# Performance work log

Hardware: AMD Instinct MI355X
Metric: run time of the kernel (lower is better)

Reference implementation:

```python
import jax, jax.numpy as jnp
import numpy as np

N_RBF = 20
CUTOFF = 5.0
N_BASIS = 128
N_FILTERS = 128
N_LAYERS = 3
B, N = 128, 128
N_PAIRS = 524288


def ssp(x):
    # ShiftedSoftplus: softplus(x) - log(2)
    return jax.nn.softplus(x) - jnp.log(2.0).astype(x.dtype)


def gaussian_rbf(d):
    # schnetpack-style GaussianRBF: offsets in [0, cutoff], shared width
    offsets = jnp.linspace(0.0, CUTOFF, N_RBF, dtype=d.dtype)
    width = offsets[1] - offsets[0]
    coeff = -0.5 / (width * width)
    diff = d[:, None] - offsets[None, :]  # [n_pairs, n_rbf]
    return jnp.exp(coeff * diff * diff)


def cosine_cutoff(d):
    fc = 0.5 * (jnp.cos(d * (jnp.pi / CUTOFF)) + 1.0)
    return fc * (d < CUTOFF).astype(d.dtype)


def setup_inputs() -> dict:
    key = jax.random.key(0)
    ks = jax.random.split(key, 16)
    inp = {
        "Z": jax.random.randint(ks[0], (B, N), 0, 100),
        "R": jax.random.normal(ks[1], (B, N, 3), dtype=jnp.float32) * 2.0,
        "idx_i": jax.random.randint(ks[2], (N_PAIRS,), 0, B * N),
        "idx_j": jax.random.randint(ks[3], (N_PAIRS,), 0, B * N),
        "emb": jax.random.normal(ks[4], (100, N_BASIS), dtype=jnp.float32) * 0.1,
    }
    s = 0.05
    inp["in2f_W"] = jax.random.normal(ks[5], (N_LAYERS, N_BASIS, N_FILTERS), dtype=jnp.float32) * s
    inp["in2f_b"] = jnp.zeros((N_LAYERS, N_FILTERS), dtype=jnp.float32)
    inp["fW1"] = jax.random.normal(ks[6], (N_LAYERS, N_RBF, N_FILTERS), dtype=jnp.float32) * s
    inp["fb1"] = jnp.zeros((N_LAYERS, N_FILTERS), dtype=jnp.float32)
    inp["fW2"] = jax.random.normal(ks[7], (N_LAYERS, N_FILTERS, N_FILTERS), dtype=jnp.float32) * s
    inp["fb2"] = jnp.zeros((N_LAYERS, N_FILTERS), dtype=jnp.float32)
    inp["oW1"] = jax.random.normal(ks[8], (N_LAYERS, N_FILTERS, N_BASIS), dtype=jnp.float32) * s
    inp["ob1"] = jnp.zeros((N_LAYERS, N_BASIS), dtype=jnp.float32)
    inp["oW2"] = jax.random.normal(ks[9], (N_LAYERS, N_BASIS, N_BASIS), dtype=jnp.float32) * s
    inp["ob2"] = jnp.zeros((N_LAYERS, N_BASIS), dtype=jnp.float32)
    return inp


def _interaction(x, f_ij, rcut_ij, idx_i, idx_j, W_in, b_in, fW1, fb1, fW2, fb2, oW1, ob1, oW2, ob2):
    # x: [B, N, n_atom_basis]
    h = jnp.einsum("bnf,fg->bng", x, W_in) + b_in          # input_to_feature
    h = h.reshape(-1, h.shape[-1])                           # [B*N, n_filters]
    # filter network on RBFs
    Wij = ssp(f_ij @ fW1 + fb1) @ fW2 + fb2                  # [n_pairs, n_filters]
    Wij = Wij * rcut_ij[:, None]
    x_ij = h[idx_j] * Wij                                     # gather + multiply
    agg = jax.ops.segment_sum(x_ij, idx_i, num_segments=h.shape[0])  # scatter_add
    out = ssp(agg @ oW1 + ob1) @ oW2 + ob2                    # feature_to_output
    return out.reshape(x.shape[0], x.shape[1], N_BASIS)


def reference(Z, R, idx_i, idx_j, emb, in2f_W, in2f_b, fW1, fb1, fW2, fb2, oW1, ob1, oW2, ob2):
    coords = R.reshape(-1, 3)                                 # [B*N, 3]
    vec = coords[idx_i] - coords[idx_j]
    d_ij = jnp.linalg.norm(vec, axis=-1)                      # [n_pairs]
    f_ij = gaussian_rbf(d_ij)                                 # [n_pairs, 20]
    rcut_ij = cosine_cutoff(d_ij)                             # [n_pairs]
    x = emb[Z]                                                # [B, N, 128]
    for l in range(N_LAYERS):
        v = _interaction(x, f_ij, rcut_ij, idx_i, idx_j,
                         in2f_W[l], in2f_b[l], fW1[l], fb1[l], fW2[l], fb2[l],
                         oW1[l], ob1[l], oW2[l], ob2[l])
        x = x + v
    return x
```

## Files before the change

kernel.cpp:

```cpp
#include <hip/hip_runtime.h>
#include <hip/hip_fp16.h>

#define NPAIRS 524288
#define NATOMS 16384
#define TBINS  2048
#define TROWS  2049
#define CAP    80
#define CUTOFF_F 5.0f

typedef _Float16 f16;
typedef f16 f16x4 __attribute__((ext_vector_type(4)));
typedef f16 f16x8 __attribute__((ext_vector_type(8)));
typedef float f32x4 __attribute__((ext_vector_type(4)));

__device__ __forceinline__ float sspf(float v) {
  float a = fabsf(v);
  return fmaxf(v, 0.0f) + log1pf(expf(-a)) - 0.69314718055994531f;
}

__device__ __forceinline__ int swz(int row, int kh) {
  return (row << 8) + ((kh << 1) ^ ((row & 7) << 4));
}
__device__ __forceinline__ int swzW(int col, int kh) {
  return (col << 7) + ((kh << 1) ^ ((col & 7) << 4));
}

__device__ __forceinline__ uint4 ldtab(const f16* __restrict__ tabL, int v, int c) {
  return *(const uint4*)(tabL + ((unsigned)(v >> 14) << 7) + (c << 3));
}
__device__ __forceinline__ uint4 ldh(const f16* __restrict__ hin, int v, int c) {
  return *(const uint4*)(hin + ((unsigned)(v & 16383) << 7) + (c << 3));
}
__device__ __forceinline__ void dot8(float* acc, uint4 wv, uint4 hv) {
  const __half* wp = (const __half*)&wv;
  const __half* hp = (const __half*)&hv;
  #pragma unroll
  for (int q = 0; q < 8; ++q)
    acc[q] = fmaf(__half2float(wp[q]), __half2float(hp[q]), acc[q]);
}

__global__ __launch_bounds__(256) void prep(const float* __restrict__ fW1,
                                            const float* __restrict__ fb1,
                                            const float* __restrict__ fW2,
                                            const float* __restrict__ fb2,
                                            f16* __restrict__ table,
                                            const float* __restrict__ in2f_W,
                                            const float* __restrict__ oW1,
                                            const float* __restrict__ oW2,
                                            f16* __restrict__ wsw,
                                            int* __restrict__ cursor) {
  __shared__ float hid[8 * 128];
  int t = threadIdx.x;
  int bid = blockIdx.x;

  if (bid >= 843) { cursor[(bid - 843) * 256 + t] = 0; return; }

  if (bid >= 771) {
    int bid2 = bid - 771;
    int mm = bid2 >> 3;
    int tloc = (bid2 & 7) * 256 + t;
    int col = tloc & 127, k0 = (tloc >> 7) << 3;
    const float* src = mm < 3 ? in2f_W + (size_t)mm * 16384
                     : mm < 6 ? oW1 + (size_t)(mm - 3) * 16384
                              : oW2 + (size_t)(mm - 6) * 16384;
    f16x8 v;
    #pragma unroll
    for (int kk = 0; kk < 8; ++kk) v[kk] = (f16)src[(k0 + kk) * 128 + col];
    *(f16x8*)((char*)wsw + (size_t)mm * 32768 + (k0 >> 6) * 16384 + swzW(col, k0 & 63)) = v;
    return;
  }

  int l = bid / 257, rem = bid % 257;
  int e = t >> 5, q = t & 31;
  int ti = rem * 8 + e;
  const float* W1 = fW1 + (size_t)l * 20 * 128;
  const float* B1 = fb1 + (size_t)l * 128;
  const float* W2 = fW2 + (size_t)l * 128 * 128;
  const float* B2 = fb2 + (size_t)l * 128;

  const float width = CUTOFF_F / 19.0f;
  const float coeff = -0.5f / (width * width);
  const float dstep = CUTOFF_F / (float)TBINS;
  float d = (float)ti * dstep;

  float4 h4 = *(const float4*)&B1[q * 4];
  #pragma unroll
  for (int r = 0; r < 20; ++r) {
    float diff = d - (float)r * width;
    float fr = expf(coeff * diff * diff);
    float4 w4 = *(const float4*)&W1[r * 128 + q * 4];
    h4.x += fr * w4.x; h4.y += fr * w4.y; h4.z += fr * w4.z; h4.w += fr * w4.w;
  }
  *(float4*)&hid[e * 128 + q * 4] =
      make_float4(sspf(h4.x), sspf(h4.y), sspf(h4.z), sspf(h4.w));
  __syncthreads();

  float4 o4 = *(const float4*)&B2[q * 4];
  const float4* W2g = (const float4*)W2;
  #pragma unroll 4
  for (int g = 0; g < 128; ++g) {
    float hv = hid[e * 128 + g];
    float4 w4 = W2g[g * 32 + q];
    o4.x += hv * w4.x; o4.y += hv * w4.y; o4.z += hv * w4.z; o4.w += hv * w4.w;
  }

  if (ti < TROWS) {
    float fc = (d < CUTOFF_F) ? 0.5f * (cosf(d * 0.62831853071795865f) + 1.0f) : 0.0f;
    f16x4 hv = { (f16)(o4.x * fc), (f16)(o4.y * fc), (f16)(o4.z * fc), (f16)(o4.w * fc) };
    *(f16x4*)((f16*)table + ((size_t)l * TROWS + ti) * 128 + q * 4) = hv;
  }
}

__global__ __launch_bounds__(256) void pg0(const int* __restrict__ Z,
                                           const float* __restrict__ emb,
                                           const f16* __restrict__ Wsw,
                                           const float* __restrict__ bias,
                                           f16* __restrict__ hout,
                                           const int* __restrict__ idx_i,
                                           const int* __restrict__ idx_j,
                                           const float* __restrict__ R,
                                           int* __restrict__ cursor,
                                           int* __restrict__ pjd) {
  __shared__ char smem[49152];
  char* Al = smem;
  char* Wl = smem + 16384;
  int t = threadIdx.x;

  if (blockIdx.x < 2048) {
    int p = blockIdx.x * 256 + t;
    int i = idx_i[p], j = idx_j[p];
    float dx = R[(size_t)i*3+0] - R[(size_t)j*3+0];
    float dy = R[(size_t)i*3+1] - R[(size_t)j*3+1];
    float dz = R[(size_t)i*3+2] - R[(size_t)j*3+2];
    float d = sqrtf(dx*dx + dy*dy + dz*dz);
    if (d < CUTOFF_F) {
      int bin = __float2int_rn(d * ((float)TBINS / CUTOFF_F));
      int slot = atomicAdd(&cursor[i], 1);
      if (slot < CAP) pjd[i * CAP + slot] = j | (bin << 14);
    }
    return;
  }

  size_t rbase = (size_t)(blockIdx.x - 2048) * 64;
  #pragma unroll
  for (int i = 0; i < 8; ++i) {
    int idx = i * 256 + t;
    int r = idx >> 5, q = idx & 31;
    int z = Z[rbase + r];
    float4 v = ((const float4*)emb)[(size_t)z * 32 + q];
    f16x4 h = { (f16)v.x, (f16)v.y, (f16)v.z, (f16)v.w };
    *(f16x4*)(Al + swz(r, q * 4)) = h;
  }
  #pragma unroll
  for (int i = 0; i < 8; ++i) ((uint4*)Wl)[i * 256 + t] = ((const uint4*)Wsw)[i * 256 + t];
  __syncthreads();

  int w = t >> 6, lane = t & 63;
  int lo = lane & 15, hi = lane >> 4;
  f16x8 fa[4];
  #pragma unroll
  for (int s = 0; s < 4; ++s)
    fa[s] = *(f16x8*)(Al + swz(16 * w + lo, s * 32 + hi * 8));

  #pragma unroll
  for (int cb = 0; cb < 8; ++cb) {
    f32x4 acc = {0.0f, 0.0f, 0.0f, 0.0f};
    #pragma unroll
    for (int s = 0; s < 4; ++s) {
      f16x8 fb = *(f16x8*)(Wl + (s >> 1) * 16384 + swzW(cb * 16 + lo, (s & 1) * 32 + hi * 8));
      acc = __builtin_amdgcn_mfma_f32_16x16x32_f16(fa[s], fb, acc, 0, 0, 0);
    }
    int col = cb * 16 + lo;
    float bc = bias[col];
    #pragma unroll
    for (int j = 0; j < 4; ++j)
      hout[(rbase + 16 * w + hi * 4 + j) * 128 + col] = (f16)(acc[j] + bc);
  }
}

template <int FIRST, int HAS_NEXT>
__global__ __launch_bounds__(512, 8) void aggfuse(const int* __restrict__ pjd,
                                                  const int* __restrict__ cnt,
                                                  const f16* __restrict__ hin,
                                                  const f16* __restrict__ tabL,
                                                  const f16* __restrict__ W1sw,
                                                  const float* __restrict__ ob1,
                                                  const f16* __restrict__ W2sw,
                                                  const float* __restrict__ ob2,
                                                  const int* __restrict__ Z,
                                                  const float* __restrict__ emb,
                                                  float* __restrict__ x,
                                                  const f16* __restrict__ Wnsw,
                                                  const float* __restrict__ bn,
                                                  f16* __restrict__ hout) {
  __shared__ char smem[24576];
  char* Wl  = smem;
  char* AlT = smem + 16384;
  char* Tl  = smem + 20480;
  int tid = threadIdx.x;
  int wv = tid >> 6, lane = tid & 63;
  int s = lane >> 4, c = lane & 15;
  int rbase = blockIdx.x * 16;
  const int S = (TBINS << 14);

  {
    int a = rbase + wv * 2 + (s & 1);
    int half = s >> 1;
    int p0 = a * CAP;
    int n = min(cnt[a], CAP);
    int nh = half * 2;

    int m = (n + 3) >> 2;
    m = max(m, __shfl_xor(m, 16, 64));
    m = max(m, __shfl_xor(m, 32, 64));

    float acc[8];
    #pragma unroll
    for (int q = 0; q < 8; ++q) acc[q] = 0.0f;

    int vA  = (nh < n)     ? pjd[p0 + nh]     : S;
    int vB  = (nh + 1 < n) ? pjd[p0 + nh + 1] : S;
    int vA1 = (nh + 4 < n) ? pjd[p0 + nh + 4] : S;
    int vB1 = (nh + 5 < n) ? pjd[p0 + nh + 5] : S;
    uint4 wA = ldtab(tabL, vA, c), hA = ldh(hin, vA, c);
    uint4 wB = ldtab(tabL, vB, c), hB = ldh(hin, vB, c);

    for (int it = 0; it < m; ++it) {
      int k2 = 4 * (it + 2) + nh;
      int vA2 = (k2 < n)     ? pjd[p0 + k2]     : S;
      int vB2 = (k2 + 1 < n) ? pjd[p0 + k2 + 1] : S;
      uint4 wAn = ldtab(tabL, vA1, c), hAn = ldh(hin, vA1, c);
      uint4 wBn = ldtab(tabL, vB1, c), hBn = ldh(hin, vB1, c);
      dot8(acc, wA, hA);
      dot8(acc, wB, hB);
      wA = wAn; hA = hAn; wB = wBn; hB = hBn;
      vA1 = vA2; vB1 = vB2;
    }

    #pragma unroll
    for (int q = 0; q < 8; ++q) acc[q] += __shfl_xor(acc[q], 32, 64);

    if (s < 2) {
      int row = wv * 2 + s;
      f16x8 pk;
      #pragma unroll
      for (int q = 0; q < 8; ++q) pk[q] = (f16)acc[q];
      *(f16x8*)(AlT + swz(row, c * 8)) = pk;
    }
  }
  __syncthreads();

  int lo = c, hi = s;
  int col = wv * 16 + lo;

  float res[4];
  if (FIRST) {
    #pragma unroll
    for (int j = 0; j < 4; ++j) {
      int z = Z[rbase + hi * 4 + j];
      res[j] = emb[(size_t)z * 128 + col];
    }
  } else {
    #pragma unroll
    for (int j = 0; j < 4; ++j)
      res[j] = x[(size_t)(rbase + hi * 4 + j) * 128 + col];
  }

  {
    f16x8 fa[4];
    #pragma unroll
    for (int ss = 0; ss < 4; ++ss)
      fa[ss] = *(f16x8*)(AlT + swz(lo, ss * 32 + hi * 8));
    f32x4 acc = {0.0f, 0.0f, 0.0f, 0.0f};
    #pragma unroll
    for (int half = 0; half < 2; ++half) {
      #pragma unroll
      for (int i = 0; i < 2; ++i)
        ((uint4*)Wl)[i * 512 + tid] = ((const uint4*)W1sw)[half * 1024 + i * 512 + tid];
      __syncthreads();
      #pragma unroll
      for (int sh = 0; sh < 2; ++sh) {
        int ss = half * 2 + sh;
        f16x8 fb = *(f16x8*)(Wl + swzW(col, sh * 32 + hi * 8));
        acc = __builtin_amdgcn_mfma_f32_16x16x32_f16(fa[ss], fb, acc, 0, 0, 0);
      }
      __syncthreads();
    }
    float bc = ob1[col];
    #pragma unroll
    for (int j = 0; j < 4; ++j)
      *(f16*)(Tl + swz(hi * 4 + j, col)) = (f16)sspf(acc[j] + bc);
  }
  __syncthreads();

  {
    f32x4 acc = {0.0f, 0.0f, 0.0f, 0.0f};
    f16x8 fa[4];
    #pragma unroll
    for (int half = 0; half < 2; ++half) {
      #pragma unroll
      for (int i = 0; i < 2; ++i)
        ((uint4*)Wl)[i * 512 + tid] = ((const uint4*)W2sw)[half * 1024 + i * 512 + tid];
      __syncthreads();
      if (half == 0) {
        #pragma unroll
        for (int ss = 0; ss < 4; ++ss)
          fa[ss] = *(f16x8*)(Tl + swz(lo, ss * 32 + hi * 8));
      }
      #pragma unroll
      for (int sh = 0; sh < 2; ++sh) {
        int ss = half * 2 + sh;
        f16x8 fb = *(f16x8*)(Wl + swzW(col, sh * 32 + hi * 8));
        acc = __builtin_amdgcn_mfma_f32_16x16x32_f16(fa[ss], fb, acc, 0, 0, 0);
      }
      __syncthreads();
    }
    float bc = ob2[col];
    #pragma unroll
    for (int j = 0; j < 4; ++j) {
      int r = hi * 4 + j;
      float xn = res[j] + acc[j] + bc;
      x[(size_t)(rbase + r) * 128 + col] = xn;
      if (HAS_NEXT) *(f16*)(AlT + swz(r, col)) = (f16)xn;
    }
  }

  if (HAS_NEXT) {
    __syncthreads();
    f32x4 acc = {0.0f, 0.0f, 0.0f, 0.0f};
    f16x8 fa[4];
    #pragma unroll
    for (int half = 0; half < 2; ++half) {
      #pragma unroll
      for (int i = 0; i < 2; ++i)
        ((uint4*)Wl)[i * 512 + tid] = ((const uint4*)Wnsw)[half * 1024 + i * 512 + tid];
      __syncthreads();
      if (half == 0) {
        #pragma unroll
        for (int ss = 0; ss < 4; ++ss)
          fa[ss] = *(f16x8*)(AlT + swz(lo, ss * 32 + hi * 8));
      }
      #pragma unroll
      for (int sh = 0; sh < 2; ++sh) {
        int ss = half * 2 + sh;
        f16x8 fb = *(f16x8*)(Wl + swzW(col, sh * 32 + hi * 8));
        acc = __builtin_amdgcn_mfma_f32_16x16x32_f16(fa[ss], fb, acc, 0, 0, 0);
      }
      __syncthreads();
    }
    float bc = bn[col];
    #pragma unroll
    for (int j = 0; j < 4; ++j)
      hout[(size_t)(rbase + hi * 4 + j) * 128 + col] = (f16)(acc[j] + bc);
  }
}

extern "C" void kernel_launch(void* const* d_in, const int* in_sizes, int n_in,
                              void* d_out, int out_size, void* d_ws, size_t ws_size,
                              hipStream_t stream) {
  const int*   Z      = (const int*)d_in[0];
  const float* R      = (const float*)d_in[1];
  const int*   idx_i  = (const int*)d_in[2];
  const int*   idx_j  = (const int*)d_in[3];
  const float* emb    = (const float*)d_in[4];
  const float* in2f_W = (const float*)d_in[5];
  const float* in2f_b = (const float*)d_in[6];
  const float* fW1    = (const float*)d_in[7];
  const float* fb1    = (const float*)d_in[8];
  const float* fW2    = (const float*)d_in[9];
  const float* fb2    = (const float*)d_in[10];
  const float* oW1    = (const float*)d_in[11];
  const float* ob1    = (const float*)d_in[12];
  const float* oW2    = (const float*)d_in[13];
  const float* ob2    = (const float*)d_in[14];
  float* x = (float*)d_out;

  char* ws = (char*)d_ws;
  int*  cursor = (int*) (ws + 0x000000);
  int*  pjd    = (int*) (ws + 0x010000);
  f16*  table  = (f16*) (ws + 0x510000);
  f16*  h0     = (f16*) (ws + 0x6A0000);
  f16*  h1     = (f16*) (ws + 0xAA0000);
  f16*  wsw    = (f16*) (ws + 0xEA0000);

  prep<<<907, 256, 0, stream>>>(fW1, fb1, fW2, fb2, table, in2f_W, oW1, oW2, wsw, cursor);
  pg0<<<2304, 256, 0, stream>>>(Z, emb, wsw, in2f_b, h0, idx_i, idx_j, R, cursor, pjd);

  aggfuse<1, 1><<<NATOMS / 16, 512, 0, stream>>>(pjd, cursor, h0, table + 0 * (size_t)TROWS * 128,
                                                 wsw + 3 * 16384, ob1,
                                                 wsw + 6 * 16384, ob2,
                                                 Z, emb, x,
                                                 wsw + 1 * 16384, in2f_b + 128, h1);
  aggfuse<0, 1><<<NATOMS / 16, 512, 0, stream>>>(pjd, cursor, h1, table + 1 * (size_t)TROWS * 128,
                                                 wsw + 4 * 16384, ob1 + 128,
                                                 wsw + 7 * 16384, ob2 + 128,
                                                 Z, emb, x,
                                                 wsw + 2 * 16384, in2f_b + 256, h0);
  aggfuse<0, 0><<<NATOMS / 16, 512, 0, stream>>>(pjd, cursor, h0, table + 2 * (size_t)TROWS * 128,
                                                 wsw + 5 * 16384, ob1 + 256,
                                                 wsw + 8 * 16384, ob2 + 256,
                                                 Z, emb, x, nullptr, nullptr, nullptr);
}
```

Before: 120.4 us.

## Read MFMA weight fragments from global memory and double aggfuse block size

The staging of 128x128 weight matrices through shared memory in aggfuse and pg0 is removed. Each wave now loads its B fragments straight from the pre-swizzled global weights, relying on L1/L2 caching. aggfuse blocks grow to 1024 threads covering 32 atoms, with two 16-row halves for the dense layers. pg0 also loads embedding rows directly into registers instead of staging them in LDS. This removes many barriers and LDS copies, at the cost of more global and L2 traffic for weights and possibly lower occupancy with the larger blocks.

Measured after the change: 124.4 us. 1.03x slower.

```diff
diff --git a/kernel.cpp b/kernel.cpp
--- a/kernel.cpp
+++ b/kernel.cpp
@@ -23,6 +23,9 @@
 }
 __device__ __forceinline__ int swzW(int col, int kh) {
   return (col << 7) + ((kh << 1) ^ ((col & 7) << 4));
+}
+__device__ __forceinline__ f16x8 ldW(const f16* __restrict__ Wg, int col, int ss, int hi) {
+  return *(const f16x8*)((const char*)Wg + (ss >> 1) * 16384 + swzW(col, (ss & 1) * 32 + hi * 8));
 }
 
 __device__ __forceinline__ uint4 ldtab(const f16* __restrict__ tabL, int v, int c) {
@@ -121,9 +124,6 @@
                                            const float* __restrict__ R,
                                            int* __restrict__ cursor,
                                            int* __restrict__ pjd) {
-  __shared__ char smem[49152];
-  char* Al = smem;
-  char* Wl = smem + 16384;
   int t = threadIdx.x;
 
   if (blockIdx.x < 2048) {
@@ -142,35 +142,28 @@
   }
 
   size_t rbase = (size_t)(blockIdx.x - 2048) * 64;
-  #pragma unroll
-  for (int i = 0; i < 8; ++i) {
-    int idx = i * 256 + t;
-    int r = idx >> 5, q = idx & 31;
-    int z = Z[rbase + r];
-    float4 v = ((const float4*)emb)[(size_t)z * 32 + q];
-    f16x4 h = { (f16)v.x, (f16)v.y, (f16)v.z, (f16)v.w };
-    *(f16x4*)(Al + swz(r, q * 4)) = h;
-  }
-  #pragma unroll
-  for (int i = 0; i < 8; ++i) ((uint4*)Wl)[i * 256 + t] = ((const uint4*)Wsw)[i * 256 + t];
-  __syncthreads();
-
   int w = t >> 6, lane = t & 63;
   int lo = lane & 15, hi = lane >> 4;
+
+  int z = Z[rbase + 16 * w + lo];
+  const float* erow = emb + (size_t)z * 128;
   f16x8 fa[4];
   #pragma unroll
-  for (int s = 0; s < 4; ++s)
-    fa[s] = *(f16x8*)(Al + swz(16 * w + lo, s * 32 + hi * 8));
+  for (int ss = 0; ss < 4; ++ss) {
+    float4 a = *(const float4*)(erow + ss * 32 + hi * 8);
+    float4 b = *(const float4*)(erow + ss * 32 + hi * 8 + 4);
+    f16x8 v = { (f16)a.x, (f16)a.y, (f16)a.z, (f16)a.w,
+                (f16)b.x, (f16)b.y, (f16)b.z, (f16)b.w };
+    fa[ss] = v;
+  }
 
   #pragma unroll
   for (int cb = 0; cb < 8; ++cb) {
+    int col = cb * 16 + lo;
     f32x4 acc = {0.0f, 0.0f, 0.0f, 0.0f};
     #pragma unroll
-    for (int s = 0; s < 4; ++s) {
-      f16x8 fb = *(f16x8*)(Wl + (s >> 1) * 16384 + swzW(cb * 16 + lo, (s & 1) * 32 + hi * 8));
-      acc = __builtin_amdgcn_mfma_f32_16x16x32_f16(fa[s], fb, acc, 0, 0, 0);
-    }
-    int col = cb * 16 + lo;
+    for (int ss = 0; ss < 4; ++ss)
+      acc = __builtin_amdgcn_mfma_f32_16x16x32_f16(fa[ss], ldW(Wsw, col, ss, hi), acc, 0, 0, 0);
     float bc = bias[col];
     #pragma unroll
     for (int j = 0; j < 4; ++j)
@@ -179,28 +172,27 @@
 }
 
 template <int FIRST, int HAS_NEXT>
-__global__ __launch_bounds__(512, 8) void aggfuse(const int* __restrict__ pjd,
-                                                  const int* __restrict__ cnt,
-                                                  const f16* __restrict__ hin,
-                                                  const f16* __restrict__ tabL,
-                                                  const f16* __restrict__ W1sw,
-                                                  const float* __restrict__ ob1,
-                                                  const f16* __restrict__ W2sw,
-                                                  const float* __restrict__ ob2,
-                                                  const int* __restrict__ Z,
-                                                  const float* __restrict__ emb,
-                                                  float* __restrict__ x,
-                                                  const f16* __restrict__ Wnsw,
-                                                  const float* __restrict__ bn,
-                                                  f16* __restrict__ hout) {
-  __shared__ char smem[24576];
-  char* Wl  = smem;
-  char* AlT = smem + 16384;
-  char* Tl  = smem + 20480;
+__global__ __launch_bounds__(1024, 8) void aggfuse(const int* __restrict__ pjd,
+                                                   const int* __restrict__ cnt,
+                                                   const f16* __restrict__ hin,
+                                                   const f16* __restrict__ tabL,
+                                                   const f16* __restrict__ W1g,
+                                                   const float* __restrict__ ob1,
+                                                   const f16* __restrict__ W2g,
+                                                   const float* __restrict__ ob2,
+                                                   const int* __restrict__ Z,
+                                                   const float* __restrict__ emb,
+                                                   float* __restrict__ x,
+                                                   const f16* __restrict__ Wng,
+                                                   const float* __restrict__ bn,
+                                                   f16* __restrict__ hout) {
+  __shared__ char smem[16384];
+  char* AlT = smem;
+  char* Tl  = smem + 8192;
   int tid = threadIdx.x;
   int wv = tid >> 6, lane = tid & 63;
   int s = lane >> 4, c = lane & 15;
-  int rbase = blockIdx.x * 16;
+  int rbase = blockIdx.x * 32;
   const int S = (TBINS << 14);
 
   {
@@ -251,74 +243,47 @@
   __syncthreads();
 
   int lo = c, hi = s;
-  int col = wv * 16 + lo;
+  int col = (wv & 7) * 16 + lo;
+  int rb16 = (wv >> 3) * 16;
 
   float res[4];
   if (FIRST) {
     #pragma unroll
     for (int j = 0; j < 4; ++j) {
-      int z = Z[rbase + hi * 4 + j];
+      int z = Z[rbase + rb16 + hi * 4 + j];
       res[j] = emb[(size_t)z * 128 + col];
     }
   } else {
     #pragma unroll
     for (int j = 0; j < 4; ++j)
-      res[j] = x[(size_t)(rbase + hi * 4 + j) * 128 + col];
-  }
-
-  {
-    f16x8 fa[4];
-    #pragma unroll
-    for (int ss = 0; ss < 4; ++ss)
-      fa[ss] = *(f16x8*)(AlT + swz(lo, ss * 32 + hi * 8));
-    f32x4 acc = {0.0f, 0.0f, 0.0f, 0.0f};
-    #pragma unroll
-    for (int half = 0; half < 2; ++half) {
-      #pragma unroll
-      for (int i = 0; i < 2; ++i)
-        ((uint4*)Wl)[i * 512 + tid] = ((const uint4*)W1sw)[half * 1024 + i * 512 + tid];
-      __syncthreads();
-      #pragma unroll
-      for (int sh = 0; sh < 2; ++sh) {
-        int ss = half * 2 + sh;
-        f16x8 fb = *(f16x8*)(Wl + swzW(col, sh * 32 + hi * 8));
-        acc = __builtin_amdgcn_mfma_f32_16x16x32_f16(fa[ss], fb, acc, 0, 0, 0);
-      }
-      __syncthreads();
-    }
-    float bc = ob1[col];
-    #pragma unroll
-    for (int j = 0; j < 4; ++j)
-      *(f16*)(Tl + swz(hi * 4 + j, col)) = (f16)sspf(acc[j] + bc);
-  }
-  __syncthreads();
+      res[j] = x[(size_t)(rbase + rb16 + hi * 4 + j) * 128 + col];
+  }
 
   {
     f32x4 acc = {0.0f, 0.0f, 0.0f, 0.0f};
-    f16x8 fa[4];
-    #pragma unroll
-    for (int half = 0; half < 2; ++half) {
-      #pragma unroll
-      for (int i = 0; i < 2; ++i)
-        ((uint4*)Wl)[i * 512 + tid] = ((const uint4*)W2sw)[half * 1024 + i * 512 + tid];
-      __syncthreads();
-      if (half == 0) {
-        #pragma unroll
-        for (int ss = 0; ss < 4; ++ss)
-          fa[ss] = *(f16x8*)(Tl + swz(lo, ss * 32 + hi * 8));
-      }
-      #pragma unroll
-      for (int sh = 0; sh < 2; ++sh) {
-        int ss = half * 2 + sh;
-        f16x8 fb = *(f16x8*)(Wl + swzW(col, sh * 32 + hi * 8));
-        acc = __builtin_amdgcn_mfma_f32_16x16x32_f16(fa[ss], fb, acc, 0, 0, 0);
-      }
-      __syncthreads();
+    #pragma unroll
+    for (int ss = 0; ss < 4; ++ss) {
+      f16x8 fa = *(f16x8*)(AlT + swz(rb16 + lo, ss * 32 + hi * 8));
+      acc = __builtin_amdgcn_mfma_f32_16x16x32_f16(fa, ldW(W1g, col, ss, hi), acc, 0, 0, 0);
+    }
+    float bc = ob1[col];
+    #pragma unroll
+    for (int j = 0; j < 4; ++j)
+      *(f16*)(Tl + swz(rb16 + hi * 4 + j, col)) = (f16)sspf(acc[j] + bc);
+  }
+  __syncthreads();
+
+  {
+    f32x4 acc = {0.0f, 0.0f, 0.0f, 0.0f};
+    #pragma unroll
+    for (int ss = 0; ss < 4; ++ss) {
+      f16x8 fa = *(f16x8*)(Tl + swz(rb16 + lo, ss * 32 + hi * 8));
+      acc = __builtin_amdgcn_mfma_f32_16x16x32_f16(fa, ldW(W2g, col, ss, hi), acc, 0, 0, 0);
     }
     float bc = ob2[col];
     #pragma unroll
     for (int j = 0; j < 4; ++j) {
-      int r = hi * 4 + j;
+      int r = rb16 + hi * 4 + j;
       float xn = res[j] + acc[j] + bc;
       x[(size_t)(rbase + r) * 128 + col] = xn;
       if (HAS_NEXT) *(f16*)(AlT + swz(r, col)) = (f16)xn;
@@ -328,30 +293,15 @@
   if (HAS_NEXT) {
     __syncthreads();
     f32x4 acc = {0.0f, 0.0f, 0.0f, 0.0f};
-    f16x8 fa[4];
-    #pragma unroll
-    for (int half = 0; half < 2; ++half) {
-      #pragma unroll
-      for (int i = 0; i < 2; ++i)
-        ((uint4*)Wl)[i * 512 + tid] = ((const uint4*)Wnsw)[half * 1024 + i * 512 + tid];
-      __syncthreads();
-      if (half == 0) {
-        #pragma unroll
-        for (int ss = 0; ss < 4; ++ss)
-          fa[ss] = *(f16x8*)(AlT + swz(lo, ss * 32 + hi * 8));
-      }
-      #pragma unroll
-      for (int sh = 0; sh < 2; ++sh) {
-        int ss = half * 2 + sh;
-        f16x8 fb = *(f16x8*)(Wl + swzW(col, sh * 32 + hi * 8));
-        acc = __builtin_amdgcn_mfma_f32_16x16x32_f16(fa[ss], fb, acc, 0, 0, 0);
-      }
-      __syncthreads();
+    #pragma unroll
+    for (int ss = 0; ss < 4; ++ss) {
+      f16x8 fa = *(f16x8*)(AlT + swz(rb16 + lo, ss * 32 + hi * 8));
+      acc = __builtin_amdgcn_mfma_f32_16x16x32_f16(fa, ldW(Wng, col, ss, hi), acc, 0, 0, 0);
     }
     float bc = bn[col];
     #pragma unroll
     for (int j = 0; j < 4; ++j)
-      hout[(size_t)(rbase + hi * 4 + j) * 128 + col] = (f16)(acc[j] + bc);
+      hout[(size_t)(rbase + rb16 + hi * 4 + j) * 128 + col] = (f16)(acc[j] + bc);
   }
 }
 
@@ -386,18 +336,18 @@
   prep<<<907, 256, 0, stream>>>(fW1, fb1, fW2, fb2, table, in2f_W, oW1, oW2, wsw, cursor);
   pg0<<<2304, 256, 0, stream>>>(Z, emb, wsw, in2f_b, h0, idx_i, idx_j, R, cursor, pjd);
 
-  aggfuse<1, 1><<<NATOMS / 16, 512, 0, stream>>>(pjd, cursor, h0, table + 0 * (size_t)TROWS * 128,
-                                                 wsw + 3 * 16384, ob1,
-                                                 wsw + 6 * 16384, ob2,
-                                                 Z, emb, x,
-                                                 wsw + 1 * 16384, in2f_b + 128, h1);
-  aggfuse<0, 1><<<NATOMS / 16, 512, 0, stream>>>(pjd, cursor, h1, table + 1 * (size_t)TROWS * 128,
-                                                 wsw + 4 * 16384, ob1 + 128,
-                                                 wsw + 7 * 16384, ob2 + 128,
-                                                 Z, emb, x,
-                                                 wsw + 2 * 16384, in2f_b + 256, h0);
-  aggfuse<0, 0><<<NATOMS / 16, 512, 0, stream>>>(pjd, cursor, h0, table + 2 * (size_t)TROWS * 128,
-                                                 wsw + 5 * 16384, ob1 + 256,
-                                                 wsw + 8 * 16384, ob2 + 256,
-                                                 Z, emb, x, nullptr, nullptr, nullptr);
-}
+  aggfuse<1, 1><<<NATOMS / 32, 1024, 0, stream>>>(pjd, cursor, h0, table + 0 * (size_t)TROWS * 128,
+                                                  wsw + 3 * 16384, ob1,
+                                                  wsw + 6 * 16384, ob2,
+                                                  Z, emb, x,
+                                                  wsw + 1 * 16384, in2f_b + 128, h1);
+  aggfuse<0, 1><<<NATOMS / 32, 1024, 0, stream>>>(pjd, cursor, h1, table + 1 * (size_t)TROWS * 128,
+                                                  wsw + 4 * 16384, ob1 + 128,
+                                                  wsw + 7 * 16384, ob2 + 128,
+                                                  Z, emb, x,
+                                                  wsw + 2 * 16384, in2f_b + 256, h0);
+  aggfuse<0, 0><<<NATOMS / 32, 1024, 0, stream>>>(pjd, cursor, h0, table + 2 * (size_t)TROWS * 128,
+                                                  wsw + 5 * 16384, ob1 + 256,
+                                                  wsw + 8 * 16384, ob2 + 256,
+                                                  Z, emb, x, nullptr, nullptr, nullptr);
+}
```
